# Optimization experiments

Measured on AMD Instinct MI355X. Metric: run time of the kernel, lower is better.

The kernel has to match this reference:

```python
import jax, jax.numpy as jnp
import numpy as np

N_NODES = 100000
N_EDGES = 3200000
IN_DIM = 128
HID = 64
OUT_DIM = 1


def gcn_conv(x, src, dst, W, b, n_nodes):
    # PyG GCNConv: h = X W; out = D^{-1/2} (A+I) D^{-1/2} h + b
    # (src, dst already include self-loops)
    h = x @ W  # [N, F_out]
    ones = jnp.ones(src.shape[0], dtype=x.dtype)
    deg = jax.ops.segment_sum(ones, dst, num_segments=n_nodes)  # in-degree with self-loops
    dinv = jnp.where(deg > 0, jax.lax.rsqrt(deg), 0.0)
    norm = dinv[src] * dinv[dst]  # [E]
    msg = h[src] * norm[:, None]  # [E, F_out] gather + scale
    agg = jax.ops.segment_sum(msg, dst, num_segments=n_nodes)  # scatter-add
    return agg + b


def setup_inputs() -> dict:
    key = jax.random.key(0)
    k = jax.random.split(key, 8)
    x = jax.random.normal(k[0], (N_NODES, IN_DIM), dtype=jnp.float32)
    edge_index = jax.random.randint(k[1], (2, N_EDGES), 0, N_NODES, dtype=jnp.int32)
    # Glorot-ish init for weights
    W1 = jax.random.normal(k[2], (IN_DIM, HID), dtype=jnp.float32) / np.sqrt(IN_DIM)
    b1 = jnp.zeros((HID,), dtype=jnp.float32)
    W2 = jax.random.normal(k[3], (HID, HID), dtype=jnp.float32) / np.sqrt(HID)
    b2 = jnp.zeros((HID,), dtype=jnp.float32)
    Wfc = jax.random.normal(k[4], (HID, OUT_DIM), dtype=jnp.float32) / np.sqrt(HID)
    bfc = jnp.zeros((OUT_DIM,), dtype=jnp.float32)
    return {"x": x, "edge_index": edge_index, "W1": W1, "b1": b1,
            "W2": W2, "b2": b2, "Wfc": Wfc, "bfc": bfc}


def reference(x, edge_index, W1, b1, W2, b2, Wfc, bfc):
    n = x.shape[0]
    loops = jnp.arange(n, dtype=edge_index.dtype)
    src = jnp.concatenate([edge_index[0], loops])
    dst = jnp.concatenate([edge_index[1], loops])
    h = jax.nn.relu(gcn_conv(x, src, dst, W1, b1, n))
    # dropout p=0.2 is identity in eval mode
    h = jax.nn.relu(gcn_conv(h, src, dst, W2, b2, n))
    out = h @ Wfc + bfc
    return jax.nn.sigmoid(out)
```

## Files before the change

kernel.cpp:

```cpp
#include <hip/hip_runtime.h>

#define INDIM 128
#define HIDD 64
#define BSHIFT 6
#define BNODES 64
#define BCAP 4096
#define MAXBUCK 2048
#define CHUNK 8192
#define ATHREADS 512
#define BPT (MAXBUCK / ATHREADS)

typedef float f32x2 __attribute__((ext_vector_type(2)));
using short8 = __attribute__((ext_vector_type(8))) short;
using f32x4  = __attribute__((ext_vector_type(4))) float;

__device__ inline unsigned short f2bf(float f) {
    unsigned u = __float_as_uint(f);
    return (unsigned short)((u + 0x7fff + ((u >> 16) & 1)) >> 16);
}
__device__ inline float bflo(unsigned v) { return __uint_as_float(v << 16); }
__device__ inline unsigned cvtpk(float a, float b) {
    unsigned r;
    asm("v_cvt_pk_bf16_f32 %0, %1, %2" : "=v"(r) : "v"(a), "v"(b));
    return r;
}


__global__ __launch_bounds__(ATHREADS) void k_bucketA(
        const int* __restrict__ srcA, const int* __restrict__ dstA,
        int* __restrict__ bcnt, unsigned* __restrict__ bucketBuf,
        int E, int N, int NBUCK) {
    __shared__ int cnt[MAXBUCK];
    __shared__ int cur[MAXBUCK];
    __shared__ unsigned short gbase[MAXBUCK];
    __shared__ unsigned short stage[CHUNK];
    __shared__ int dLds[CHUNK];
    __shared__ int wsum[ATHREADS / 64];
    int t = threadIdx.x;
    int EV = E + N;
    int begin = blockIdx.x * CHUNK;
    int end = begin + CHUNK;
    if (end > EV) end = EV;
    if (begin >= EV) return;
    int nLoc = end - begin;

    for (int b = t; b < MAXBUCK; b += ATHREADS) cnt[b] = 0;
    __syncthreads();

    for (int i = begin + t; i < end; i += ATHREADS) {
        int d = (i < E) ? dstA[i] : (i - E);
        dLds[i - begin] = d;
        atomicAdd(&cnt[d >> BSHIFT], 1);
    }
    __syncthreads();

    int vq[BPT];
    int psum = 0;
#pragma unroll
    for (int q = 0; q < BPT; ++q) { vq[q] = cnt[t * BPT + q]; psum += vq[q]; }
    int lane = t & 63, w = t >> 6;
    int s = psum;
#pragma unroll
    for (int off = 1; off < 64; off <<= 1) {
        int u = __shfl_up(s, off, 64);
        if (lane >= off) s += u;
    }
    if (lane == 63) wsum[w] = s;
    __syncthreads();
    if (t < ATHREADS / 64) {
        int x = wsum[t];
#pragma unroll
        for (int off = 1; off < ATHREADS / 64; off <<= 1) {
            int u = __shfl_up(x, off, 64);
            if (t >= off) x += u;
        }
        wsum[t] = x;
    }
    __syncthreads();
    int run = ((w > 0) ? wsum[w - 1] : 0) + s - psum;
#pragma unroll
    for (int q = 0; q < BPT; ++q) {
        cur[t * BPT + q] = run;
        run += vq[q];
    }

    int b0 = (int)(((unsigned)blockIdx.x * 683u) % (unsigned)NBUCK);
    for (int idx = t; idx < NBUCK; idx += ATHREADS) {
        int b = idx + b0;
        if (b >= NBUCK) b -= NBUCK;
        int c = cnt[b];
        gbase[b] = (unsigned short)((c > 0) ? atomicAdd(&bcnt[b], c) : 0);
    }
    __syncthreads();

    for (int j = t; j < nLoc; j += ATHREADS) {
        int d = dLds[j];
        int slot = atomicAdd(&cur[d >> BSHIFT], 1);
        stage[slot] = (unsigned short)j;
    }
    __syncthreads();

    for (int j = t; j < nLoc; j += ATHREADS) {
        int loc = (int)stage[j];
        int d = dLds[loc];
        int i2 = begin + loc;
        int s2 = (i2 < E) ? srcA[i2] : d;
        int b = d >> BSHIFT;
        int local = j - (cur[b] - cnt[b]);
        int slot = (int)gbase[b] + local;
        if (slot < BCAP)
            bucketBuf[(size_t)b * BCAP + slot] = ((unsigned)s2 << BSHIFT) | (d & (BNODES - 1));
    }
}

__global__ __launch_bounds__(512) void k_scanbuck(const int* __restrict__ bcnt,
                                                  int* __restrict__ bstart,
                                                  int* __restrict__ rowStartN,
                                                  int NBUCK) {
    __shared__ int wsum[8];
    int t = threadIdx.x;
    int v[4];
    int psum = 0;
#pragma unroll
    for (int q = 0; q < 4; ++q) {
        int b = t * 4 + q;
        v[q] = (b < NBUCK) ? bcnt[b] : 0;
        psum += v[q];
    }
    int lane = t & 63, w = t >> 6;
    int s = psum;
#pragma unroll
    for (int off = 1; off < 64; off <<= 1) {
        int u = __shfl_up(s, off, 64);
        if (lane >= off) s += u;
    }
    if (lane == 63) wsum[w] = s;
    __syncthreads();
    if (t < 8) {
        int x = wsum[t];
#pragma unroll
        for (int off = 1; off < 8; off <<= 1) {
            int u = __shfl_up(x, off, 64);
            if (t >= off) x += u;
        }
        wsum[t] = x;
    }
    __syncthreads();
    int run = ((w > 0) ? wsum[w - 1] : 0) + s - psum;
#pragma unroll
    for (int q = 0; q < 4; ++q) {
        int b = t * 4 + q;
        if (b < NBUCK) bstart[b] = run;
        run += v[q];
    }
    if (t == 511) *rowStartN = run;
}

__global__ __launch_bounds__(256) void k_fillB(
        const int* __restrict__ bcnt, const unsigned* __restrict__ bucketBuf,
        const int* __restrict__ bstart, int* __restrict__ rowStart,
        float* __restrict__ dinv, int* __restrict__ srcList, int N) {
    __shared__ int cnt[BNODES];
    __shared__ int cur[BNODES];
    __shared__ unsigned stage[BCAP];
    int b = blockIdx.x;
    int t = threadIdx.x;
    if (t < BNODES) cnt[t] = 0;
    __syncthreads();
    int n = bcnt[b];
    if (n > BCAP) n = BCAP;
    int base = bstart[b];
    const unsigned* buf = bucketBuf + (size_t)b * BCAP;
    for (int e = t; e < n; e += 256)
        atomicAdd(&cnt[buf[e] & (BNODES - 1)], 1);
    __syncthreads();
    if (t < BNODES) {
        int c = cnt[t];
        int s = c;
#pragma unroll
        for (int off = 1; off < BNODES; off <<= 1) {
            int u = __shfl_up(s, off, 64);
            if (t >= off) s += u;
        }
        int excl = s - c;
        cur[t] = excl;
        int node = b * BNODES + t;
        if (node < N) {
            rowStart[node] = base + excl;
            dinv[node] = rsqrtf((float)c);
        }
    }
    __syncthreads();
    for (int e = t; e < n; e += 256) {
        unsigned entry = buf[e];
        int slot = atomicAdd(&cur[entry & (BNODES - 1)], 1);
        stage[slot] = entry;
    }
    __syncthreads();
    for (int j = t; j < n; j += 256)
        srcList[base + j] = (int)(stage[j] >> BSHIFT);
}

template <int K, bool F32IN>
__global__ __launch_bounds__(256) void k_gemm_mfma(const void* __restrict__ Xv,
                                                   const float* __restrict__ W,
                                                   const float* __restrict__ dinv,
                                                   unsigned short* __restrict__ Hs,
                                                   int N) {
    __shared__ unsigned short AH[64][72];
    __shared__ unsigned short AL[64][72];
    __shared__ unsigned short BH[64][72];
    __shared__ unsigned short BL[64][72];
    int t = threadIdx.x;
    int row0 = blockIdx.x * 64;
    if (F32IN && blockIdx.x == 0 && t < 32)
        ((unsigned*)Hs)[(size_t)N * 32 + t] = 0u;
    int w = t >> 6, lane = t & 63;
    int lr = lane & 15, lh = lane >> 4;
    f32x4 acc[4];
#pragma unroll
    for (int tn = 0; tn < 4; ++tn) acc[tn] = (f32x4){0.f, 0.f, 0.f, 0.f};

    for (int kb = 0; kb < K; kb += 64) {
        if (kb) __syncthreads();
        if constexpr (F32IN) {
            const float* X = (const float*)Xv;
#pragma unroll
            for (int qq = 0; qq < 4; ++qq) {
                int f = qq * 256 + t;
                int r = f >> 4, c4 = (f & 15) << 2;
                int row = row0 + r;
                float4 x = make_float4(0.f, 0.f, 0.f, 0.f);
                if (row < N) x = *(const float4*)&X[(size_t)row * K + kb + c4];
                unsigned u01 = cvtpk(x.x, x.y), u23 = cvtpk(x.z, x.w);
                float l0 = x.x - bflo(u01);
                float l1 = x.y - __uint_as_float(u01 & 0xffff0000u);
                float l2 = x.z - bflo(u23);
                float l3 = x.w - __uint_as_float(u23 & 0xffff0000u);
                unsigned v01 = cvtpk(l0, l1), v23 = cvtpk(l2, l3);
                *(uint2*)&AH[r][c4] = make_uint2(u01, u23);
                *(uint2*)&AL[r][c4] = make_uint2(v01, v23);
            }
        } else {
            const unsigned* X = (const unsigned*)Xv;
#pragma unroll
            for (int qq = 0; qq < 2; ++qq) {
                int f = qq * 256 + t;
                int r = f >> 3, c8 = (f & 7) << 3;
                int row = row0 + r;
                uint4 v = make_uint4(0u, 0u, 0u, 0u);
                if (row < N) v = *(const uint4*)&X[(size_t)row * 32 + (c8 >> 1)];
                *(uint4*)&AH[r][c8] = v;
            }
        }
        {
            int n = (t & 15) + ((t >> 6) << 4);
            int kc0 = ((t >> 4) & 3) << 2;
#pragma unroll
            for (int qq = 0; qq < 4; ++qq) {
                int kc = kc0 + (qq << 4);
                float w0 = W[(size_t)(kb + kc + 0) * HIDD + n];
                float w1 = W[(size_t)(kb + kc + 1) * HIDD + n];
                float w2 = W[(size_t)(kb + kc + 2) * HIDD + n];
                float w3 = W[(size_t)(kb + kc + 3) * HIDD + n];
                unsigned u01 = cvtpk(w0, w1), u23 = cvtpk(w2, w3);
                float l0 = w0 - bflo(u01);
                float l1 = w1 - __uint_as_float(u01 & 0xffff0000u);
                float l2 = w2 - bflo(u23);
                float l3 = w3 - __uint_as_float(u23 & 0xffff0000u);
                unsigned v01 = cvtpk(l0, l1), v23 = cvtpk(l2, l3);
                *(uint2*)&BH[n][kc] = make_uint2(u01, u23);
                *(uint2*)&BL[n][kc] = make_uint2(v01, v23);
            }
        }
        __syncthreads();
#pragma unroll
        for (int s = 0; s < 2; ++s) {
            short8 ah = *(const short8*)&AH[16 * w + lr][32 * s + 8 * lh];
#pragma unroll
            for (int tn = 0; tn < 4; ++tn) {
                short8 bh = *(const short8*)&BH[16 * tn + lr][32 * s + 8 * lh];
                short8 bl = *(const short8*)&BL[16 * tn + lr][32 * s + 8 * lh];
                acc[tn] = __builtin_amdgcn_mfma_f32_16x16x32_bf16(ah, bh, acc[tn], 0, 0, 0);
                acc[tn] = __builtin_amdgcn_mfma_f32_16x16x32_bf16(ah, bl, acc[tn], 0, 0, 0);
                if constexpr (F32IN) {
                    short8 al = *(const short8*)&AL[16 * w + lr][32 * s + 8 * lh];
                    acc[tn] = __builtin_amdgcn_mfma_f32_16x16x32_bf16(al, bh, acc[tn], 0, 0, 0);
                }
            }
        }
    }
    int rb = row0 + 16 * w + 4 * lh;
#pragma unroll
    for (int r = 0; r < 4; ++r) {
        int row = rb + r;
        if (row < N) {
            float di = dinv[row];
#pragma unroll
            for (int tn = 0; tn < 4; ++tn)
                Hs[(size_t)row * HIDD + 16 * tn + lr] = f2bf(acc[tn][r] * di);
        }
    }
}


#define PK2(accH, accL, u0, u1)                                              \
    do {                                                                     \
        f32x2 hh_, ll_;                                                      \
        hh_.x = __uint_as_float(u0);                                         \
        hh_.y = __uint_as_float(u1);                                         \
        ll_.x = __uint_as_float((u0) << 16);                                 \
        ll_.y = __uint_as_float((u1) << 16);                                 \
        asm("v_pk_add_f32 %0, %1, %0" : "+v"(accH) : "v"(hh_));              \
        asm("v_pk_add_f32 %0, %1, %0" : "+v"(accL) : "v"(ll_));              \
    } while (0)

#define ACC4(H0, L0, H1, L1, v4)                                             \
    do { PK2(H0, L0, (v4).x, (v4).y); PK2(H1, L1, (v4).z, (v4).w); } while (0)

#define ROWG(sidx) (*(const uint4*)(Hb + (((unsigned)(sidx) << 7) + qb)))

#define SRC6(P, ebeg, eend)                                                  \
    int P##b = (ebeg) + g;                                                   \
    int P##s0 = (P##b      < (eend)) ? srcList[P##b]      : N;               \
    int P##s1 = (P##b + 8  < (eend)) ? srcList[P##b + 8]  : N;               \
    int P##s2 = (P##b + 16 < (eend)) ? srcList[P##b + 16] : N;               \
    int P##s3 = (P##b + 24 < (eend)) ? srcList[P##b + 24] : N;               \
    int P##s4 = (P##b + 32 < (eend)) ? srcList[P##b + 32] : N;               \
    int P##s5 = (P##b + 40 < (eend)) ? srcList[P##b + 40] : N

#define GATH6(P)                                                             \
    uint4 P##v0 = ROWG(P##s0); uint4 P##v1 = ROWG(P##s1);                    \
    uint4 P##v2 = ROWG(P##s2); uint4 P##v3 = ROWG(P##s3);                    \
    uint4 P##v4 = ROWG(P##s4); uint4 P##v5 = ROWG(P##s5)

#define ACC6(P, H0, L0, H1, L1)                                              \
    do { ACC4(H0, L0, H1, L1, P##v0); ACC4(H0, L0, H1, L1, P##v1);           \
         ACC4(H0, L0, H1, L1, P##v2); ACC4(H0, L0, H1, L1, P##v3);           \
         ACC4(H0, L0, H1, L1, P##v4); ACC4(H0, L0, H1, L1, P##v5); } while (0)

#define BIGLOOP(ePos, eEnd, H0, L0, H1, L1)                                  \
    while ((eEnd) - (ePos) > 48) {                    \
        int s0 = srcList[(ePos) + g];                                        \
        int s1 = srcList[(ePos) + 8 + g];                                    \
        int s2 = srcList[(ePos) + 16 + g];                                   \
        int s3 = srcList[(ePos) + 24 + g];                                   \
        uint4 v0 = ROWG(s0); uint4 v1 = ROWG(s1);                            \
        uint4 v2 = ROWG(s2); uint4 v3 = ROWG(s3);                            \
        ACC4(H0, L0, H1, L1, v0); ACC4(H0, L0, H1, L1, v1);                  \
        ACC4(H0, L0, H1, L1, v2); ACC4(H0, L0, H1, L1, v3);                  \
        (ePos) += 32;                                                        \
    }

#define AGG_PAIR(HPTR)                                                       \
    const char* Hb = (const char*)(HPTR);                                    \
    unsigned qb = (unsigned)q << 4;                                          \
    int2 ra = *(const int2*)&rowStart[i0];                                   \
    int rc = rowStart[i0 + 2];                                               \
    int beg0 = ra.x, end0 = ra.y;                                            \
    int beg1 = (i1 == i0) ? ra.x : ra.y;                                     \
    int end1 = (i1 == i0) ? ra.y : rc;                                       \
    f32x2 h0A = {0.f,0.f}, l0A = {0.f,0.f}, h1A = {0.f,0.f}, l1A = {0.f,0.f};\
    f32x2 h0B = {0.f,0.f}, l0B = {0.f,0.f}, h1B = {0.f,0.f}, l1B = {0.f,0.f};\
    int e0 = beg0, e1 = beg1;                                                \
    BIGLOOP(e0, end0, h0A, l0A, h1A, l1A)                                    \
    BIGLOOP(e1, end1, h0B, l0B, h1B, l1B)                                    \
    SRC6(A, e0, end0);                                                       \
    SRC6(B, e1, end1);                                                       \
    GATH6(A);                                                                \
    GATH6(B);                                                                \
    ACC6(A, h0A, l0A, h1A, l1A);                                             \
    ACC6(B, h0B, l0B, h1B, l1B);                                             \
    float v8A[8] = {l0A.x, h0A.x, l0A.y, h0A.y, l1A.x, h1A.x, l1A.y, h1A.y}; \
    float v8B[8] = {l0B.x, h0B.x, l0B.y, h0B.y, l1B.x, h1B.x, l1B.y, h1B.y}; \
    _Pragma("unroll")                                                        \
    for (int k = 0; k < 8; ++k) {                                            \
        v8A[k] += __shfl_xor(v8A[k], 8, 64);                                 \
        v8A[k] += __shfl_xor(v8A[k], 16, 64);                                 \
        v8A[k] += __shfl_xor(v8A[k], 32, 64);                                 \
        v8B[k] += __shfl_xor(v8B[k], 8, 64);                                 \
        v8B[k] += __shfl_xor(v8B[k], 16, 64);                                 \
        v8B[k] += __shfl_xor(v8B[k], 32, 64);                                 \
    }

__global__ __launch_bounds__(256) void k_agg_relu(
        const unsigned* __restrict__ Hs, const float* __restrict__ dinv,
        const int* __restrict__ rowStart, const int* __restrict__ srcList,
        const float* __restrict__ bias, unsigned* __restrict__ O, int N) {
    int wid  = (blockIdx.x * blockDim.x + threadIdx.x) >> 6;
    int lane = threadIdx.x & 63;
    int i0 = 2 * wid;
    if (i0 >= N) return;
    i0 = __builtin_amdgcn_readfirstlane(i0);
    int i1 = (i0 + 1 < N) ? i0 + 1 : i0;
    int g = lane >> 3;
    int q = lane & 7;
    AGG_PAIR(Hs)
    if (g < 2) {
        int io = g ? i1 : i0;
        float u0 = g ? v8B[0] : v8A[0];
        float u1 = g ? v8B[1] : v8A[1];
        float u2 = g ? v8B[2] : v8A[2];
        float u3 = g ? v8B[3] : v8A[3];
        float u4 = g ? v8B[4] : v8A[4];
        float u5 = g ? v8B[5] : v8A[5];
        float u6 = g ? v8B[6] : v8A[6];
        float u7 = g ? v8B[7] : v8A[7];
        float di = dinv[io];
        float4 ba = *(const float4*)&bias[q * 8];
        float4 bb = *(const float4*)&bias[q * 8 + 4];
        const float* bp = (const float*)&ba;
        const float* bq = (const float*)&bb;
        float r0 = fmaxf(di * u0 + bp[0], 0.f);
        float r1 = fmaxf(di * u1 + bp[1], 0.f);
        float r2 = fmaxf(di * u2 + bp[2], 0.f);
        float r3 = fmaxf(di * u3 + bp[3], 0.f);
        float r4 = fmaxf(di * u4 + bq[0], 0.f);
        float r5 = fmaxf(di * u5 + bq[1], 0.f);
        float r6 = fmaxf(di * u6 + bq[2], 0.f);
        float r7 = fmaxf(di * u7 + bq[3], 0.f);
        uint4 o;
        o.x = cvtpk(r0, r1);
        o.y = cvtpk(r2, r3);
        o.z = cvtpk(r4, r5);
        o.w = cvtpk(r6, r7);
        *(uint4*)(O + (size_t)io * 32 + q * 4) = o;
    }
}

__global__ __launch_bounds__(256) void k_agg_fc(
        const unsigned* __restrict__ Hs, const float* __restrict__ dinv,
        const int* __restrict__ rowStart, const int* __restrict__ srcList,
        const float* __restrict__ b2, const float* __restrict__ Wfc,
        const float* __restrict__ bfc, float* __restrict__ out, int N) {
    int wid  = (blockIdx.x * blockDim.x + threadIdx.x) >> 6;
    int lane = threadIdx.x & 63;
    int i0 = 2 * wid;
    if (i0 >= N) return;
    i0 = __builtin_amdgcn_readfirstlane(i0);
    int i1 = (i0 + 1 < N) ? i0 + 1 : i0;
    int g = lane >> 3;
    int q = lane & 7;
    AGG_PAIR(Hs)
    if (g < 2) {
        int io = g ? i1 : i0;
        float u0 = g ? v8B[0] : v8A[0];
        float u1 = g ? v8B[1] : v8A[1];
        float u2 = g ? v8B[2] : v8A[2];
        float u3 = g ? v8B[3] : v8A[3];
        float u4 = g ? v8B[4] : v8A[4];
        float u5 = g ? v8B[5] : v8A[5];
        float u6 = g ? v8B[6] : v8A[6];
        float u7 = g ? v8B[7] : v8A[7];
        float di = dinv[io];
        float4 ba = *(const float4*)&b2[q * 8];
        float4 bb = *(const float4*)&b2[q * 8 + 4];
        float4 wa = *(const float4*)&Wfc[q * 8];
        float4 wb = *(const float4*)&Wfc[q * 8 + 4];
        const float* bp = (const float*)&ba;
        const float* bq = (const float*)&bb;
        const float* wp = (const float*)&wa;
        const float* wq = (const float*)&wb;
        float p = fmaxf(di * u0 + bp[0], 0.f) * wp[0]
                + fmaxf(di * u1 + bp[1], 0.f) * wp[1]
                + fmaxf(di * u2 + bp[2], 0.f) * wp[2]
                + fmaxf(di * u3 + bp[3], 0.f) * wp[3]
                + fmaxf(di * u4 + bq[0], 0.f) * wq[0]
                + fmaxf(di * u5 + bq[1], 0.f) * wq[1]
                + fmaxf(di * u6 + bq[2], 0.f) * wq[2]
                + fmaxf(di * u7 + bq[3], 0.f) * wq[3];
        p += __shfl_xor(p, 1, 64);
        p += __shfl_xor(p, 2, 64);
        p += __shfl_xor(p, 4, 64);
        if (q == 0) {
            float z = p + bfc[0];
            out[io] = 1.f / (1.f + __expf(-z));
        }
    }
}


extern "C" void kernel_launch(void* const* d_in, const int* in_sizes, int n_in,
                              void* d_out, int out_size, void* d_ws, size_t ws_size,
                              hipStream_t stream) {
    const float* x   = (const float*)d_in[0];
    const int*   ei  = (const int*)d_in[1];
    const float* W1  = (const float*)d_in[2];
    const float* b1  = (const float*)d_in[3];
    const float* W2  = (const float*)d_in[4];
    const float* b2  = (const float*)d_in[5];
    const float* Wfc = (const float*)d_in[6];
    const float* bfc = (const float*)d_in[7];
    float* out = (float*)d_out;

    int N  = in_sizes[0] / INDIM;
    int E  = in_sizes[1] / 2;
    int EV = E + N;
    const int* srcA = ei;
    const int* dstA = ei + E;

    int NBUCK = (N + BNODES - 1) / BNODES;
    size_t bucketBytes = (size_t)NBUCK * BCAP * 4;
    size_t hsBytes     = (size_t)(N + 1) * HIDD * 2;

    char* ws = (char*)d_ws;
    size_t off = 0;
    auto alloc = [&](size_t bytes) -> char* {
        char* p = ws + off;
        off = (off + bytes + 255) & ~(size_t)255;
        return p;
    };
    int*   rowStart = (int*)alloc((size_t)(N + 9) * 4);
    float* dinv     = (float*)alloc((size_t)N * 4);
    int*   bcnt     = (int*)alloc((size_t)NBUCK * 4);
    int*   bstart   = (int*)alloc((size_t)NBUCK * 4);
    int*   srcList  = (int*)alloc((size_t)(EV + 48) * 4);
    char*  region   = alloc(bucketBytes > hsBytes ? bucketBytes : hsBytes);
    unsigned*       bucketBuf = (unsigned*)region;
    unsigned short* Hs        = (unsigned short*)region;
    unsigned* bufB = (unsigned*)alloc(hsBytes);

    hipMemsetAsync(bcnt, 0, (size_t)NBUCK * 4, stream);
    int aBlocks = (EV + CHUNK - 1) / CHUNK;
    hipLaunchKernelGGL(k_bucketA, dim3(aBlocks), dim3(ATHREADS), 0, stream,
                       srcA, dstA, bcnt, bucketBuf, E, N, NBUCK);
    hipLaunchKernelGGL(k_scanbuck, dim3(1), dim3(512), 0, stream,
                       bcnt, bstart, rowStart + N, NBUCK);
    hipLaunchKernelGGL(k_fillB, dim3(NBUCK), dim3(256), 0, stream,
                       bcnt, bucketBuf, bstart, rowStart, dinv, srcList, N);

    int gBlocks = (N + 63) / 64;
    hipLaunchKernelGGL((k_gemm_mfma<INDIM, true>), dim3(gBlocks), dim3(256), 0, stream,
                       (const void*)x, W1, dinv, Hs, N);

    int aggWaves  = (N + 1) / 2;
    int aggBlocks = (aggWaves + 3) / 4;
    hipLaunchKernelGGL(k_agg_relu, dim3(aggBlocks), dim3(256), 0, stream,
                       (const unsigned*)Hs, dinv, rowStart, srcList, b1, bufB, N);

    hipLaunchKernelGGL((k_gemm_mfma<HIDD, false>), dim3(gBlocks), dim3(256), 0, stream,
                       (const void*)bufB, W2, dinv, Hs, N);

    hipLaunchKernelGGL(k_agg_fc, dim3(aggBlocks), dim3(256), 0, stream,
                       (const unsigned*)Hs, dinv, rowStart, srcList, b2, Wfc, bfc, out, N);
}
```

Measured before the change: 175.6 us.

## Fuse layer-2 GEMM into first aggregation kernel and add nontemporal loads

The first aggregation kernel now applies bias and ReLU, then multiplies each node pair by W2 with MFMA directly from registers. It writes the dinv-scaled H2 in bf16, so the separate second GEMM launch and the intermediate activation round-trip go away. W2 is split into hi/lo bf16 parts in shared memory in every block. This adds per-block setup work and runs MFMAs with only 2 of 16 rows used. Nontemporal load and store hints are also added to the edge-index, srcList, X and output accesses.

```diff
diff --git a/kernel.cpp b/kernel.cpp
--- a/kernel.cpp
+++ b/kernel.cpp
@@ -13,6 +13,9 @@
 typedef float f32x2 __attribute__((ext_vector_type(2)));
 using short8 = __attribute__((ext_vector_type(8))) short;
 using f32x4  = __attribute__((ext_vector_type(4))) float;
+using f4v    = __attribute__((ext_vector_type(4))) float;
+
+#define NTL(P) __builtin_nontemporal_load(P)
 
 __device__ inline unsigned short f2bf(float f) {
     unsigned u = __float_as_uint(f);
@@ -48,7 +51,7 @@
     __syncthreads();
 
     for (int i = begin + t; i < end; i += ATHREADS) {
-        int d = (i < E) ? dstA[i] : (i - E);
+        int d = (i < E) ? NTL(dstA + i) : (i - E);
         dLds[i - begin] = d;
         atomicAdd(&cnt[d >> BSHIFT], 1);
     }
@@ -104,7 +107,7 @@
         int loc = (int)stage[j];
         int d = dLds[loc];
         int i2 = begin + loc;
-        int s2 = (i2 < E) ? srcA[i2] : d;
+        int s2 = (i2 < E) ? NTL(srcA + i2) : d;
         int b = d >> BSHIFT;
         int local = j - (cur[b] - cnt[b]);
         int slot = (int)gbase[b] + local;
@@ -201,8 +204,8 @@
         srcList[base + j] = (int)(stage[j] >> BSHIFT);
 }
 
-template <int K, bool F32IN>
-__global__ __launch_bounds__(256) void k_gemm_mfma(const void* __restrict__ Xv,
+template <int K>
+__global__ __launch_bounds__(256) void k_gemm_mfma(const float* __restrict__ X,
                                                    const float* __restrict__ W,
                                                    const float* __restrict__ dinv,
                                                    unsigned short* __restrict__ Hs,
@@ -213,7 +216,7 @@
     __shared__ unsigned short BL[64][72];
     int t = threadIdx.x;
     int row0 = blockIdx.x * 64;
-    if (F32IN && blockIdx.x == 0 && t < 32)
+    if (blockIdx.x == 0 && t < 32)
         ((unsigned*)Hs)[(size_t)N * 32 + t] = 0u;
     int w = t >> 6, lane = t & 63;
     int lr = lane & 15, lh = lane >> 4;
@@ -223,35 +226,21 @@
 
     for (int kb = 0; kb < K; kb += 64) {
         if (kb) __syncthreads();
-        if constexpr (F32IN) {
-            const float* X = (const float*)Xv;
-#pragma unroll
-            for (int qq = 0; qq < 4; ++qq) {
-                int f = qq * 256 + t;
-                int r = f >> 4, c4 = (f & 15) << 2;
-                int row = row0 + r;
-                float4 x = make_float4(0.f, 0.f, 0.f, 0.f);
-                if (row < N) x = *(const float4*)&X[(size_t)row * K + kb + c4];
-                unsigned u01 = cvtpk(x.x, x.y), u23 = cvtpk(x.z, x.w);
-                float l0 = x.x - bflo(u01);
-                float l1 = x.y - __uint_as_float(u01 & 0xffff0000u);
-                float l2 = x.z - bflo(u23);
-                float l3 = x.w - __uint_as_float(u23 & 0xffff0000u);
-                unsigned v01 = cvtpk(l0, l1), v23 = cvtpk(l2, l3);
-                *(uint2*)&AH[r][c4] = make_uint2(u01, u23);
-                *(uint2*)&AL[r][c4] = make_uint2(v01, v23);
-            }
-        } else {
-            const unsigned* X = (const unsigned*)Xv;
-#pragma unroll
-            for (int qq = 0; qq < 2; ++qq) {
-                int f = qq * 256 + t;
-                int r = f >> 3, c8 = (f & 7) << 3;
-                int row = row0 + r;
-                uint4 v = make_uint4(0u, 0u, 0u, 0u);
-                if (row < N) v = *(const uint4*)&X[(size_t)row * 32 + (c8 >> 1)];
-                *(uint4*)&AH[r][c8] = v;
-            }
+#pragma unroll
+        for (int qq = 0; qq < 4; ++qq) {
+            int f = qq * 256 + t;
+            int r = f >> 4, c4 = (f & 15) << 2;
+            int row = row0 + r;
+            f4v x = {0.f, 0.f, 0.f, 0.f};
+            if (row < N) x = NTL((const f4v*)&X[(size_t)row * K + kb + c4]);
+            unsigned u01 = cvtpk(x[0], x[1]), u23 = cvtpk(x[2], x[3]);
+            float l0 = x[0] - bflo(u01);
+            float l1 = x[1] - __uint_as_float(u01 & 0xffff0000u);
+            float l2 = x[2] - bflo(u23);
+            float l3 = x[3] - __uint_as_float(u23 & 0xffff0000u);
+            unsigned v01 = cvtpk(l0, l1), v23 = cvtpk(l2, l3);
+            *(uint2*)&AH[r][c4] = make_uint2(u01, u23);
+            *(uint2*)&AL[r][c4] = make_uint2(v01, v23);
         }
         {
             int n = (t & 15) + ((t >> 6) << 4);
@@ -277,16 +266,14 @@
 #pragma unroll
         for (int s = 0; s < 2; ++s) {
             short8 ah = *(const short8*)&AH[16 * w + lr][32 * s + 8 * lh];
+            short8 al = *(const short8*)&AL[16 * w + lr][32 * s + 8 * lh];
 #pragma unroll
             for (int tn = 0; tn < 4; ++tn) {
                 short8 bh = *(const short8*)&BH[16 * tn + lr][32 * s + 8 * lh];
                 short8 bl = *(const short8*)&BL[16 * tn + lr][32 * s + 8 * lh];
                 acc[tn] = __builtin_amdgcn_mfma_f32_16x16x32_bf16(ah, bh, acc[tn], 0, 0, 0);
                 acc[tn] = __builtin_amdgcn_mfma_f32_16x16x32_bf16(ah, bl, acc[tn], 0, 0, 0);
-                if constexpr (F32IN) {
-                    short8 al = *(const short8*)&AL[16 * w + lr][32 * s + 8 * lh];
-                    acc[tn] = __builtin_amdgcn_mfma_f32_16x16x32_bf16(al, bh, acc[tn], 0, 0, 0);
-                }
+                acc[tn] = __builtin_amdgcn_mfma_f32_16x16x32_bf16(al, bh, acc[tn], 0, 0, 0);
             }
         }
     }
@@ -322,12 +309,12 @@
 
 #define SRC6(P, ebeg, eend)                                                  \
     int P##b = (ebeg) + g;                                                   \
-    int P##s0 = (P##b      < (eend)) ? srcList[P##b]      : N;               \
-    int P##s1 = (P##b + 8  < (eend)) ? srcList[P##b + 8]  : N;               \
-    int P##s2 = (P##b + 16 < (eend)) ? srcList[P##b + 16] : N;               \
-    int P##s3 = (P##b + 24 < (eend)) ? srcList[P##b + 24] : N;               \
-    int P##s4 = (P##b + 32 < (eend)) ? srcList[P##b + 32] : N;               \
-    int P##s5 = (P##b + 40 < (eend)) ? srcList[P##b + 40] : N
+    int P##s0 = (P##b      < (eend)) ? NTL(srcList + P##b)      : N;         \
+    int P##s1 = (P##b + 8  < (eend)) ? NTL(srcList + P##b + 8)  : N;         \
+    int P##s2 = (P##b + 16 < (eend)) ? NTL(srcList + P##b + 16) : N;         \
+    int P##s3 = (P##b + 24 < (eend)) ? NTL(srcList + P##b + 24) : N;         \
+    int P##s4 = (P##b + 32 < (eend)) ? NTL(srcList + P##b + 32) : N;         \
+    int P##s5 = (P##b + 40 < (eend)) ? NTL(srcList + P##b + 40) : N
 
 #define GATH6(P)                                                             \
     uint4 P##v0 = ROWG(P##s0); uint4 P##v1 = ROWG(P##s1);                    \
@@ -341,10 +328,10 @@
 
 #define BIGLOOP(ePos, eEnd, H0, L0, H1, L1)                                  \
     while ((eEnd) - (ePos) > 48) {                    \
-        int s0 = srcList[(ePos) + g];                                        \
-        int s1 = srcList[(ePos) + 8 + g];                                    \
-        int s2 = srcList[(ePos) + 16 + g];                                   \
-        int s3 = srcList[(ePos) + 24 + g];                                   \
+        int s0 = NTL(srcList + (ePos) + g);                                  \
+        int s1 = NTL(srcList + (ePos) + 8 + g);                              \
+        int s2 = NTL(srcList + (ePos) + 16 + g);                             \
+        int s3 = NTL(srcList + (ePos) + 24 + g);                             \
         uint4 v0 = ROWG(s0); uint4 v1 = ROWG(s1);                            \
         uint4 v2 = ROWG(s2); uint4 v3 = ROWG(s3);                            \
         ACC4(H0, L0, H1, L1, v0); ACC4(H0, L0, H1, L1, v1);                  \
@@ -383,12 +370,33 @@
         v8B[k] += __shfl_xor(v8B[k], 32, 64);                                 \
     }
 
-__global__ __launch_bounds__(256) void k_agg_relu(
+__global__ __launch_bounds__(256) void k_agg_g2(
         const unsigned* __restrict__ Hs, const float* __restrict__ dinv,
         const int* __restrict__ rowStart, const int* __restrict__ srcList,
-        const float* __restrict__ bias, unsigned* __restrict__ O, int N) {
-    int wid  = (blockIdx.x * blockDim.x + threadIdx.x) >> 6;
-    int lane = threadIdx.x & 63;
+        const float* __restrict__ b1, const float* __restrict__ W2,
+        unsigned short* __restrict__ H2, int N) {
+    __shared__ unsigned short w2h[64][72];
+    __shared__ unsigned short w2l[64][72];
+    int t = threadIdx.x;
+    for (int idx = t; idx < 1024; idx += 256) {
+        int k = idx >> 4, n4 = (idx & 15) << 2;
+        f4v v = NTL((const f4v*)&W2[k * 64 + n4]);
+#pragma unroll
+        for (int e2 = 0; e2 < 4; ++e2) {
+            float wv = v[e2];
+            unsigned short hu = f2bf(wv);
+            float wh = __uint_as_float((unsigned)hu << 16);
+            unsigned short lu = f2bf(wv - wh);
+            w2h[n4 + e2][k] = hu;
+            w2l[n4 + e2][k] = lu;
+        }
+    }
+    if (blockIdx.x == 0 && t < 32)
+        ((unsigned*)H2)[(size_t)N * 32 + t] = 0u;
+    __syncthreads();
+
+    int wid  = (blockIdx.x * blockDim.x + t) >> 6;
+    int lane = t & 63;
     int i0 = 2 * wid;
     if (i0 >= N) return;
     i0 = __builtin_amdgcn_readfirstlane(i0);
@@ -396,35 +404,47 @@
     int g = lane >> 3;
     int q = lane & 7;
     AGG_PAIR(Hs)
-    if (g < 2) {
-        int io = g ? i1 : i0;
-        float u0 = g ? v8B[0] : v8A[0];
-        float u1 = g ? v8B[1] : v8A[1];
-        float u2 = g ? v8B[2] : v8A[2];
-        float u3 = g ? v8B[3] : v8A[3];
-        float u4 = g ? v8B[4] : v8A[4];
-        float u5 = g ? v8B[5] : v8A[5];
-        float u6 = g ? v8B[6] : v8A[6];
-        float u7 = g ? v8B[7] : v8A[7];
-        float di = dinv[io];
-        float4 ba = *(const float4*)&bias[q * 8];
-        float4 bb = *(const float4*)&bias[q * 8 + 4];
-        const float* bp = (const float*)&ba;
-        const float* bq = (const float*)&bb;
-        float r0 = fmaxf(di * u0 + bp[0], 0.f);
-        float r1 = fmaxf(di * u1 + bp[1], 0.f);
-        float r2 = fmaxf(di * u2 + bp[2], 0.f);
-        float r3 = fmaxf(di * u3 + bp[3], 0.f);
-        float r4 = fmaxf(di * u4 + bq[0], 0.f);
-        float r5 = fmaxf(di * u5 + bq[1], 0.f);
-        float r6 = fmaxf(di * u6 + bq[2], 0.f);
-        float r7 = fmaxf(di * u7 + bq[3], 0.f);
-        uint4 o;
-        o.x = cvtpk(r0, r1);
-        o.y = cvtpk(r2, r3);
-        o.z = cvtpk(r4, r5);
-        o.w = cvtpk(r6, r7);
-        *(uint4*)(O + (size_t)io * 32 + q * 4) = o;
+
+    float diA = dinv[i0], diB = dinv[i1];
+    int m = lane & 15, hi4 = lane >> 4;
+    f32x4 acc2[4];
+#pragma unroll
+    for (int tn = 0; tn < 4; ++tn) acc2[tn] = (f32x4){0.f, 0.f, 0.f, 0.f};
+#pragma unroll
+    for (int s = 0; s < 2; ++s) {
+        int kq = 4 * s + hi4;
+        float pA[8], pB[8];
+#pragma unroll
+        for (int j = 0; j < 8; ++j) {
+            float sA = __shfl(v8A[j], kq, 64);
+            float sB = __shfl(v8B[j], kq, 64);
+            float bj = b1[8 * kq + j];
+            pA[j] = fmaxf(fmaf(diA, sA, bj), 0.f);
+            pB[j] = fmaxf(fmaf(diB, sB, bj), 0.f);
+        }
+        union { unsigned u[4]; short8 s8; } af;
+#pragma unroll
+        for (int jj = 0; jj < 4; ++jj) {
+            float e0 = (m == 0) ? pA[2 * jj]     : (m == 1 ? pB[2 * jj]     : 0.f);
+            float e1 = (m == 0) ? pA[2 * jj + 1] : (m == 1 ? pB[2 * jj + 1] : 0.f);
+            af.u[jj] = cvtpk(e0, e1);
+        }
+#pragma unroll
+        for (int tn = 0; tn < 4; ++tn) {
+            short8 bh = *(const short8*)&w2h[16 * tn + m][32 * s + 8 * hi4];
+            short8 bl = *(const short8*)&w2l[16 * tn + m][32 * s + 8 * hi4];
+            acc2[tn] = __builtin_amdgcn_mfma_f32_16x16x32_bf16(af.s8, bh, acc2[tn], 0, 0, 0);
+            acc2[tn] = __builtin_amdgcn_mfma_f32_16x16x32_bf16(af.s8, bl, acc2[tn], 0, 0, 0);
+        }
+    }
+    if (hi4 == 0) {
+#pragma unroll
+        for (int tn = 0; tn < 4; ++tn) {
+            __builtin_nontemporal_store(f2bf(acc2[tn][0] * diA),
+                                        &H2[(size_t)i0 * HIDD + 16 * tn + m]);
+            __builtin_nontemporal_store(f2bf(acc2[tn][1] * diB),
+                                        &H2[(size_t)i1 * HIDD + 16 * tn + m]);
+        }
     }
 }
 
@@ -474,7 +494,7 @@
         p += __shfl_xor(p, 4, 64);
         if (q == 0) {
             float z = p + bfc[0];
-            out[io] = 1.f / (1.f + __expf(-z));
+            __builtin_nontemporal_store(1.f / (1.f + __expf(-z)), &out[io]);
         }
     }
 }
@@ -518,7 +538,7 @@
     char*  region   = alloc(bucketBytes > hsBytes ? bucketBytes : hsBytes);
     unsigned*       bucketBuf = (unsigned*)region;
     unsigned short* Hs        = (unsigned short*)region;
-    unsigned* bufB = (unsigned*)alloc(hsBytes);
+    unsigned short* H2 = (unsigned short*)alloc(hsBytes);
 
     hipMemsetAsync(bcnt, 0, (size_t)NBUCK * 4, stream);
     int aBlocks = (EV + CHUNK - 1) / CHUNK;
@@ -530,17 +550,14 @@
                        bcnt, bucketBuf, bstart, rowStart, dinv, srcList, N);
 
     int gBlocks = (N + 63) / 64;
-    hipLaunchKernelGGL((k_gemm_mfma<INDIM, true>), dim3(gBlocks), dim3(256), 0, stream,
-                       (const void*)x, W1, dinv, Hs, N);
+    hipLaunchKernelGGL((k_gemm_mfma<INDIM>), dim3(gBlocks), dim3(256), 0, stream,
+                       x, W1, dinv, Hs, N);
 
     int aggWaves  = (N + 1) / 2;
     int aggBlocks = (aggWaves + 3) / 4;
-    hipLaunchKernelGGL(k_agg_relu, dim3(aggBlocks), dim3(256), 0, stream,
-                       (const unsigned*)Hs, dinv, rowStart, srcList, b1, bufB, N);
-
-    hipLaunchKernelGGL((k_gemm_mfma<HIDD, false>), dim3(gBlocks), dim3(256), 0, stream,
-                       (const void*)bufB, W2, dinv, Hs, N);
+    hipLaunchKernelGGL(k_agg_g2, dim3(aggBlocks), dim3(256), 0, stream,
+                       (const unsigned*)Hs, dinv, rowStart, srcList, b1, W2, H2, N);
 
     hipLaunchKernelGGL(k_agg_fc, dim3(aggBlocks), dim3(256), 0, stream,
-                       (const unsigned*)Hs, dinv, rowStart, srcList, b2, Wfc, bfc, out, N);
-}
+                       (const unsigned*)H2, dinv, rowStart, srcList, b2, Wfc, bfc, out, N);
+}
```

New measurement: 259.8 us. 1.48x slower.

## Use nontemporal loads for streamed data and per-wave counters in bucket fill

Applied to the files above, without the earlier changes.

Streamed edge arrays, the input feature rows and the srcList reads in the aggregation loops now use nontemporal loads, and the final output uses a nontemporal store. The intent is to keep the gathered H rows resident in cache instead of one-shot data. The bucket-fill kernel moves to 512 threads with per-wave LDS histograms and cursors, which cuts LDS atomic contention, and a single wave merges the per-wave counts into the prefix scan. The result stays deterministic only up to the order of entries within a node, and the larger blocks may lower occupancy.

```diff
diff --git a/kernel.cpp b/kernel.cpp
--- a/kernel.cpp
+++ b/kernel.cpp
@@ -9,10 +9,15 @@
 #define CHUNK 8192
 #define ATHREADS 512
 #define BPT (MAXBUCK / ATHREADS)
+#define FB_THREADS 512
+#define FB_WAVES (FB_THREADS / 64)
 
 typedef float f32x2 __attribute__((ext_vector_type(2)));
 using short8 = __attribute__((ext_vector_type(8))) short;
 using f32x4  = __attribute__((ext_vector_type(4))) float;
+using f4v    = __attribute__((ext_vector_type(4))) float;
+
+#define NTL(P) __builtin_nontemporal_load(P)
 
 __device__ inline unsigned short f2bf(float f) {
     unsigned u = __float_as_uint(f);
@@ -48,7 +53,7 @@
     __syncthreads();
 
     for (int i = begin + t; i < end; i += ATHREADS) {
-        int d = (i < E) ? dstA[i] : (i - E);
+        int d = (i < E) ? NTL(dstA + i) : (i - E);
         dLds[i - begin] = d;
         atomicAdd(&cnt[d >> BSHIFT], 1);
     }
@@ -104,7 +109,7 @@
         int loc = (int)stage[j];
         int d = dLds[loc];
         int i2 = begin + loc;
-        int s2 = (i2 < E) ? srcA[i2] : d;
+        int s2 = (i2 < E) ? NTL(srcA + i2) : d;
         int b = d >> BSHIFT;
         int local = j - (cur[b] - cnt[b]);
         int slot = (int)gbase[b] + local;
@@ -156,48 +161,53 @@
     if (t == 511) *rowStartN = run;
 }
 
-__global__ __launch_bounds__(256) void k_fillB(
+__global__ __launch_bounds__(FB_THREADS) void k_fillB(
         const int* __restrict__ bcnt, const unsigned* __restrict__ bucketBuf,
         const int* __restrict__ bstart, int* __restrict__ rowStart,
         float* __restrict__ dinv, int* __restrict__ srcList, int N) {
-    __shared__ int cnt[BNODES];
-    __shared__ int cur[BNODES];
+    __shared__ int cntw[FB_WAVES][BNODES];
+    __shared__ int curw[FB_WAVES][BNODES];
     __shared__ unsigned stage[BCAP];
     int b = blockIdx.x;
     int t = threadIdx.x;
-    if (t < BNODES) cnt[t] = 0;
+    int w = t >> 6, lane = t & 63;
+    cntw[w][lane] = 0;
     __syncthreads();
     int n = bcnt[b];
     if (n > BCAP) n = BCAP;
     int base = bstart[b];
     const unsigned* buf = bucketBuf + (size_t)b * BCAP;
-    for (int e = t; e < n; e += 256)
-        atomicAdd(&cnt[buf[e] & (BNODES - 1)], 1);
-    __syncthreads();
-    if (t < BNODES) {
-        int c = cnt[t];
-        int s = c;
+    for (int e = t; e < n; e += FB_THREADS)
+        atomicAdd(&cntw[w][buf[e] & (BNODES - 1)], 1);
+    __syncthreads();
+    if (w == 0) {
+        int tot = 0;
+        int pre[FB_WAVES];
+#pragma unroll
+        for (int ww = 0; ww < FB_WAVES; ++ww) { pre[ww] = tot; tot += cntw[ww][lane]; }
+        int s = tot;
 #pragma unroll
         for (int off = 1; off < BNODES; off <<= 1) {
             int u = __shfl_up(s, off, 64);
-            if (t >= off) s += u;
-        }
-        int excl = s - c;
-        cur[t] = excl;
-        int node = b * BNODES + t;
+            if (lane >= off) s += u;
+        }
+        int excl = s - tot;
+        int node = b * BNODES + lane;
         if (node < N) {
             rowStart[node] = base + excl;
-            dinv[node] = rsqrtf((float)c);
-        }
-    }
-    __syncthreads();
-    for (int e = t; e < n; e += 256) {
+            dinv[node] = rsqrtf((float)tot);
+        }
+#pragma unroll
+        for (int ww = 0; ww < FB_WAVES; ++ww) curw[ww][lane] = excl + pre[ww];
+    }
+    __syncthreads();
+    for (int e = t; e < n; e += FB_THREADS) {
         unsigned entry = buf[e];
-        int slot = atomicAdd(&cur[entry & (BNODES - 1)], 1);
+        int slot = atomicAdd(&curw[w][entry & (BNODES - 1)], 1);
         stage[slot] = entry;
     }
     __syncthreads();
-    for (int j = t; j < n; j += 256)
+    for (int j = t; j < n; j += FB_THREADS)
         srcList[base + j] = (int)(stage[j] >> BSHIFT);
 }
 
@@ -230,13 +240,13 @@
                 int f = qq * 256 + t;
                 int r = f >> 4, c4 = (f & 15) << 2;
                 int row = row0 + r;
-                float4 x = make_float4(0.f, 0.f, 0.f, 0.f);
-                if (row < N) x = *(const float4*)&X[(size_t)row * K + kb + c4];
-                unsigned u01 = cvtpk(x.x, x.y), u23 = cvtpk(x.z, x.w);
-                float l0 = x.x - bflo(u01);
-                float l1 = x.y - __uint_as_float(u01 & 0xffff0000u);
-                float l2 = x.z - bflo(u23);
-                float l3 = x.w - __uint_as_float(u23 & 0xffff0000u);
+                f4v x = {0.f, 0.f, 0.f, 0.f};
+                if (row < N) x = NTL((const f4v*)&X[(size_t)row * K + kb + c4]);
+                unsigned u01 = cvtpk(x[0], x[1]), u23 = cvtpk(x[2], x[3]);
+                float l0 = x[0] - bflo(u01);
+                float l1 = x[1] - __uint_as_float(u01 & 0xffff0000u);
+                float l2 = x[2] - bflo(u23);
+                float l3 = x[3] - __uint_as_float(u23 & 0xffff0000u);
                 unsigned v01 = cvtpk(l0, l1), v23 = cvtpk(l2, l3);
                 *(uint2*)&AH[r][c4] = make_uint2(u01, u23);
                 *(uint2*)&AL[r][c4] = make_uint2(v01, v23);
@@ -322,12 +332,12 @@
 
 #define SRC6(P, ebeg, eend)                                                  \
     int P##b = (ebeg) + g;                                                   \
-    int P##s0 = (P##b      < (eend)) ? srcList[P##b]      : N;               \
-    int P##s1 = (P##b + 8  < (eend)) ? srcList[P##b + 8]  : N;               \
-    int P##s2 = (P##b + 16 < (eend)) ? srcList[P##b + 16] : N;               \
-    int P##s3 = (P##b + 24 < (eend)) ? srcList[P##b + 24] : N;               \
-    int P##s4 = (P##b + 32 < (eend)) ? srcList[P##b + 32] : N;               \
-    int P##s5 = (P##b + 40 < (eend)) ? srcList[P##b + 40] : N
+    int P##s0 = (P##b      < (eend)) ? NTL(srcList + P##b)      : N;         \
+    int P##s1 = (P##b + 8  < (eend)) ? NTL(srcList + P##b + 8)  : N;         \
+    int P##s2 = (P##b + 16 < (eend)) ? NTL(srcList + P##b + 16) : N;         \
+    int P##s3 = (P##b + 24 < (eend)) ? NTL(srcList + P##b + 24) : N;         \
+    int P##s4 = (P##b + 32 < (eend)) ? NTL(srcList + P##b + 32) : N;         \
+    int P##s5 = (P##b + 40 < (eend)) ? NTL(srcList + P##b + 40) : N
 
 #define GATH6(P)                                                             \
     uint4 P##v0 = ROWG(P##s0); uint4 P##v1 = ROWG(P##s1);                    \
@@ -341,10 +351,10 @@
 
 #define BIGLOOP(ePos, eEnd, H0, L0, H1, L1)                                  \
     while ((eEnd) - (ePos) > 48) {                    \
-        int s0 = srcList[(ePos) + g];                                        \
-        int s1 = srcList[(ePos) + 8 + g];                                    \
-        int s2 = srcList[(ePos) + 16 + g];                                   \
-        int s3 = srcList[(ePos) + 24 + g];                                   \
+        int s0 = NTL(srcList + (ePos) + g);                                  \
+        int s1 = NTL(srcList + (ePos) + 8 + g);                              \
+        int s2 = NTL(srcList + (ePos) + 16 + g);                             \
+        int s3 = NTL(srcList + (ePos) + 24 + g);                             \
         uint4 v0 = ROWG(s0); uint4 v1 = ROWG(s1);                            \
         uint4 v2 = ROWG(s2); uint4 v3 = ROWG(s3);                            \
         ACC4(H0, L0, H1, L1, v0); ACC4(H0, L0, H1, L1, v1);                  \
@@ -474,7 +484,7 @@
         p += __shfl_xor(p, 4, 64);
         if (q == 0) {
             float z = p + bfc[0];
-            out[io] = 1.f / (1.f + __expf(-z));
+            __builtin_nontemporal_store(1.f / (1.f + __expf(-z)), &out[io]);
         }
     }
 }
@@ -526,7 +536,7 @@
                        srcA, dstA, bcnt, bucketBuf, E, N, NBUCK);
     hipLaunchKernelGGL(k_scanbuck, dim3(1), dim3(512), 0, stream,
                        bcnt, bstart, rowStart + N, NBUCK);
-    hipLaunchKernelGGL(k_fillB, dim3(NBUCK), dim3(256), 0, stream,
+    hipLaunchKernelGGL(k_fillB, dim3(NBUCK), dim3(FB_THREADS), 0, stream,
                        bcnt, bucketBuf, bstart, rowStart, dinv, srcList, N);
 
     int gBlocks = (N + 63) / 64;
```

Measured after the change: 218.9 us. 1.25x slower.
